# Kernel tuning notes

Measured on AMD Instinct MI355X. Metric: run time of the kernel, lower is better.

## Reference

```python
import jax, jax.numpy as jnp
import numpy as np

N = 50000
E = 800000
F_IN = 128
HID = 64
OUT = 64
H = 4
NEG_SLOPE = 0.2


def setup_inputs() -> dict:
    key = jax.random.key(0)
    ks = jax.random.split(key, 10)
    s = lambda fan_in: 1.0 / np.sqrt(fan_in)
    x = jax.random.normal(ks[0], (N, F_IN), dtype=jnp.float32)
    edge_index = jax.random.randint(ks[1], (2, E), 0, N, dtype=jnp.int64)
    # layer 1: in -> hid, heads H, concat=False
    W1 = jax.random.normal(ks[2], (F_IN, H * HID), dtype=jnp.float32) * s(F_IN)
    a_src1 = jax.random.normal(ks[3], (H, HID), dtype=jnp.float32) * s(HID)
    a_dst1 = jax.random.normal(ks[4], (H, HID), dtype=jnp.float32) * s(HID)
    b1 = jnp.zeros((HID,), dtype=jnp.float32)
    # layer 2: hid -> out
    W2 = jax.random.normal(ks[5], (HID, H * OUT), dtype=jnp.float32) * s(HID)
    a_src2 = jax.random.normal(ks[6], (H, OUT), dtype=jnp.float32) * s(OUT)
    a_dst2 = jax.random.normal(ks[7], (H, OUT), dtype=jnp.float32) * s(OUT)
    b2 = jnp.zeros((OUT,), dtype=jnp.float32)
    return {"x": x, "edge_index": edge_index, "W1": W1, "a_src1": a_src1,
            "a_dst1": a_dst1, "b1": b1, "W2": W2, "a_src2": a_src2,
            "a_dst2": a_dst2, "b2": b2}


def gat_layer(x, src, dst, W, a_s, a_d, b):
    n, h, c = x.shape[0], a_s.shape[0], a_s.shape[1]
    hfeat = (x @ W).reshape(n, h, c)                      # [N,H,C]
    # per-node attention halves, gathered per edge
    alpha_src = jnp.einsum('nhc,hc->nh', hfeat, a_s)       # [N,H]
    alpha_dst = jnp.einsum('nhc,hc->nh', hfeat, a_d)
    e = alpha_src[src] + alpha_dst[dst]                    # [E,H]
    e = jnp.where(e >= 0, e, NEG_SLOPE * e)                # LeakyReLU(0.2)
    # segment softmax over destination node neighborhoods
    m = jax.ops.segment_max(e, dst, num_segments=n)
    e = jnp.exp(e - m[dst])
    denom = jax.ops.segment_sum(e, dst, num_segments=n)
    alpha = e / (denom[dst] + 1e-16)                       # [E,H]
    msg = hfeat[src] * alpha[:, :, None]                   # [E,H,C]
    out = jax.ops.segment_sum(msg, dst, num_segments=n)    # [N,H,C]
    return out.mean(axis=1) + b                            # concat=False -> head mean


def reference(x, edge_index, W1, a_src1, a_dst1, b1, W2, a_src2, a_dst2, b2):
    src, dst = edge_index[0], edge_index[1]
    h = gat_layer(x, src, dst, W1, a_src1, a_dst1, b1)
    h = jax.nn.relu(h)
    h = gat_layer(h, src, dst, W2, a_src2, a_dst2, b2)
    return jax.nn.log_softmax(h, axis=1)
```

## Files before the change

kernel.cpp:

```cpp
#include <hip/hip_runtime.h>
#include <math.h>

constexpr int NNODE = 50000;
constexpr int FIN   = 128;
constexpr int HID   = 64;
constexpr int NH    = 4;
constexpr int NC    = 256;
constexpr float NEG = 0.2f;
constexpr int MPAD  = 50048;
constexpr int SCANB = (NNODE + 255) / 256;

typedef unsigned short u16;
typedef unsigned int   u32;
typedef __fp16 h16x8 __attribute__((ext_vector_type(8)));
typedef __fp16 h2    __attribute__((ext_vector_type(2)));
typedef float  f32x4 __attribute__((ext_vector_type(4)));

__device__ __forceinline__ u16 f2h(float f) {
  union { __fp16 h; u16 u; } c; c.h = (__fp16)f; return c.u;
}
__device__ __forceinline__ h2 u2h2(u32 u) {
  union { u32 u; h2 h; } c; c.u = u; return c.h;
}
__device__ __forceinline__ float readlane_f(float v, int l) {
  return __int_as_float(__builtin_amdgcn_readlane(__float_as_int(v), l));
}
__device__ __forceinline__ u32 h2bf8(u16 hx) {
  return ((u32)hx + 0x7Fu + ((hx >> 8) & 1u)) >> 8;
}

__global__ __launch_bounds__(256) void pack_zero(const float* __restrict__ W1,
                                                 const float* __restrict__ W2,
                                                 u16* __restrict__ Bp1, u16* __restrict__ Bp2,
                                                 int* __restrict__ deg, int packBlocks, int n) {
  int b = blockIdx.x;
  if (b < packBlocks) {
    int i = b * 256 + threadIdx.x;
    const int t1 = FIN * NC;
    const int t2 = HID * NC;
    if (i < t1) {
      int k = i >> 8, c = i & 255;
      Bp1[((size_t)(k >> 3) * 256 + c) * 8 + (k & 7)] = f2h(W1[i]);
    } else if (i < t1 + t2) {
      int j = i - t1;
      int k = j >> 8, c = j & 255;
      Bp2[((size_t)(k >> 3) * 256 + c) * 8 + (k & 7)] = f2h(W2[j]);
    }
  } else {
    int i = (b - packBlocks) * 256 + threadIdx.x;
    if (i < n) deg[i] = 0;
  }
}

__global__ __launch_bounds__(256) void scan_phase1(const int* __restrict__ deg,
                                                   int* __restrict__ blockSums, int n) {
  __shared__ int sm[256];
  int tid = threadIdx.x;
  int i = blockIdx.x * 256 + tid;
  sm[tid] = (i < n) ? deg[i] : 0;
  __syncthreads();
#pragma unroll
  for (int o = 128; o > 0; o >>= 1) {
    if (tid < o) sm[tid] += sm[tid + o];
    __syncthreads();
  }
  if (tid == 0) blockSums[blockIdx.x] = sm[0];
}

__global__ __launch_bounds__(256) void scan_phase23(const int* __restrict__ blockSums,
                                                    const int* __restrict__ deg,
                                                    int* __restrict__ offs, int n) {
  __shared__ int ss[256];
  __shared__ int sm[256];
  int tid = threadIdx.x;
  ss[tid] = (tid < SCANB) ? blockSums[tid] : 0;
  __syncthreads();
#pragma unroll
  for (int o = 1; o < 256; o <<= 1) {
    int t = (tid >= o) ? ss[tid - o] : 0;
    __syncthreads();
    ss[tid] += t;
    __syncthreads();
  }
  int blockOff = (blockIdx.x == 0) ? 0 : ss[blockIdx.x - 1];
  int i = blockIdx.x * 256 + tid;
  int v = (i < n) ? deg[i] : 0;
  sm[tid] = v;
  __syncthreads();
#pragma unroll
  for (int o = 1; o < 256; o <<= 1) {
    int t = (tid >= o) ? sm[tid - o] : 0;
    __syncthreads();
    sm[tid] += t;
    __syncthreads();
  }
  int ex = sm[tid] - v + blockOff;
  if (i < n) offs[i] = ex;
  if (blockIdx.x == SCANB - 1 && tid == 255) offs[n] = ss[SCANB - 1];
}

template <int KS, bool AF32, bool F8>
__device__ __forceinline__ void gemm_body(
    int bx, const void* __restrict__ Aptr, const u16* __restrict__ Bp,
    const float* __restrict__ a_s, const float* __restrict__ a_d,
    void* __restrict__ feat, float* __restrict__ al_s, float* __restrict__ al_d, int M) {
  const int K = 32 * KS;
  int lane = threadIdx.x & 63;
  int wv = threadIdx.x >> 6;
  int q = lane >> 4, r = lane & 15;
  int m0 = bx * 64 + wv * 16;

  h16x8 af[KS];
  if (AF32) {
    int ar = m0 + r; if (ar >= M) ar = M - 1;
    const float* arow = (const float*)Aptr + (size_t)ar * K + q * 8;
#pragma unroll
    for (int ks = 0; ks < KS; ++ks) {
      float4 v0 = *(const float4*)(arow + ks * 32);
      float4 v1 = *(const float4*)(arow + ks * 32 + 4);
      union { h16x8 v; h2 p[4]; } u;
      u.p[0] = __builtin_amdgcn_cvt_pkrtz(v0.x, v0.y);
      u.p[1] = __builtin_amdgcn_cvt_pkrtz(v0.z, v0.w);
      u.p[2] = __builtin_amdgcn_cvt_pkrtz(v1.x, v1.y);
      u.p[3] = __builtin_amdgcn_cvt_pkrtz(v1.z, v1.w);
      af[ks] = u.v;
    }
  } else {
    const u16* arow = (const u16*)Aptr + (size_t)(m0 + r) * K + q * 8;
#pragma unroll
    for (int ks = 0; ks < KS; ++ks) af[ks] = *(const h16x8*)(arow + ks * 32);
  }

  int node_base = m0 + q * 4;
  u32 pk8[4][4];
  if (F8) {
#pragma unroll
    for (int a = 0; a < 4; ++a)
#pragma unroll
      for (int b = 0; b < 4; ++b) pk8[a][b] = 0u;
  }
#pragma unroll
  for (int h = 0; h < NH; ++h) {
    f32x4 acc[4];
#pragma unroll
    for (int c4 = 0; c4 < 4; ++c4) {
      acc[c4] = (f32x4){0.f, 0.f, 0.f, 0.f};
      const u16* bp = Bp + ((size_t)q * 256 + (h * 4 + c4) * 16 + r) * 8;
#pragma unroll
      for (int ks = 0; ks < KS; ++ks) {
        h16x8 bf = *(const h16x8*)(bp + (size_t)ks * 4 * 256 * 8);
        acc[c4] = __builtin_amdgcn_mfma_f32_16x16x32_f16(af[ks], bf, acc[c4], 0, 0, 0);
      }
    }
    float ps[4] = {0.f, 0.f, 0.f, 0.f}, pd[4] = {0.f, 0.f, 0.f, 0.f};
#pragma unroll
    for (int c4 = 0; c4 < 4; ++c4) {
      float sa = a_s[h * HID + c4 * 16 + r];
      float da = a_d[h * HID + c4 * 16 + r];
#pragma unroll
      for (int reg = 0; reg < 4; ++reg) {
        float v = acc[c4][reg];
        ps[reg] += v * sa;
        pd[reg] += v * da;
        if (F8) {
          pk8[c4][reg] |= h2bf8(f2h(v)) << (8 * h);
        } else {
          int node = node_base + reg;
          if (node < M) ((u16*)feat)[(size_t)node * NC + (c4 * 16 + r) * NH + h] = f2h(v);
        }
      }
    }
#pragma unroll
    for (int reg = 0; reg < 4; ++reg) {
#pragma unroll
      for (int o = 1; o < 16; o <<= 1) {
        ps[reg] += __shfl_xor(ps[reg], o);
        pd[reg] += __shfl_xor(pd[reg], o);
      }
      int node = node_base + reg;
      if (r == 0 && node < M) {
        al_s[node * NH + h] = ps[reg];
        al_d[node * NH + h] = pd[reg];
      }
    }
  }
  if (F8) {
#pragma unroll
    for (int c4 = 0; c4 < 4; ++c4)
#pragma unroll
      for (int reg = 0; reg < 4; ++reg) {
        int node = node_base + reg;
        if (node < M)
          *(u32*)((char*)feat + (size_t)node * 256 + (c4 * 16 + r) * 4) = pk8[c4][reg];
      }
  }
}

__global__ __launch_bounds__(256) void count_gemm1(
    const float* __restrict__ x, const u16* __restrict__ Bp1,
    const float* __restrict__ a_s, const float* __restrict__ a_d,
    void* __restrict__ hf8, float* __restrict__ al_s, float* __restrict__ al_d, int M,
    const int* __restrict__ ei, int* __restrict__ deg, int* __restrict__ rank,
    int E, int gemmBlocks) {
  int b = blockIdx.x;
  if (b < gemmBlocks) {
    gemm_body<4, true, true>(b, x, Bp1, a_s, a_d, hf8, al_s, al_d, M);
  } else {
    int i = (b - gemmBlocks) * 256 + threadIdx.x;
    if (i < E) rank[i] = atomicAdd(&deg[ei[E + i]], 1);
  }
}

__global__ __launch_bounds__(256) void scatter_kernel(
    const int* __restrict__ ei, const int* __restrict__ offs,
    const int* __restrict__ rank, int* __restrict__ csr_src, int E) {
  int i = blockIdx.x * 256 + threadIdx.x;
  if (i < E) {
    int dst = ei[E + i];
    csr_src[offs[dst] + rank[i]] = ei[i];
  }
}

__global__ __launch_bounds__(256) void gemm2_kernel(
    const u16* __restrict__ h1bf, const u16* __restrict__ Bp2,
    const float* __restrict__ a_s, const float* __restrict__ a_d,
    void* __restrict__ hf8, float* __restrict__ al_s, float* __restrict__ al_d, int M) {
  gemm_body<2, false, true>(blockIdx.x, h1bf, Bp2, a_s, a_d, hf8, al_s, al_d, M);
}

template <bool FINAL, bool F8>
__global__ __launch_bounds__(256) void agg_kernel(const void* __restrict__ feat,
                                                  const float4* __restrict__ al_s4,
                                                  const float4* __restrict__ al_d4,
                                                  const int* __restrict__ offs,
                                                  const int* __restrict__ csr,
                                                  const float* __restrict__ bias,
                                                  void* __restrict__ out_v, int n) {
  int lane = threadIdx.x & 63;
  int node = blockIdx.x * 4 + (threadIdx.x >> 6);
  if (node >= n) return;
  float4 ad = al_d4[node];
  int lj = lane & 7;
  int hsel = (lane >> 3) & 3;
  float adv = hsel == 0 ? ad.x : (hsel == 1 ? ad.y : (hsel == 2 ? ad.z : ad.w));
  h2 acc01 = {(__fp16)0.f, (__fp16)0.f};
  h2 acc23 = {(__fp16)0.f, (__fp16)0.f};
  float dacc = 0.f;
  int s = offs[node], e = offs[node + 1];
  int nch = (e - s + 7) >> 3;
  int i = s;
  int voff = F8 ? lane * 4 : lane * 8;

  int vidx = 0;
  float4 as = make_float4(0.f, 0.f, 0.f, 0.f);
  uint2 hv[8];
  if (nch > 0) {
    int id0 = i + lj; if (id0 >= e) id0 = e - 1;
    vidx = csr[id0];
    as = al_s4[vidx];
#pragma unroll
    for (int j = 0; j < 8; ++j) {
      int sa = __builtin_amdgcn_readlane(vidx, j);
      if (F8) hv[j].x = *(const u32*)((const char*)feat + (size_t)sa * 256 + voff);
      else    hv[j]   = *(const uint2*)((const char*)feat + (size_t)sa * 512 + voff);
    }
  }

  for (int ch = 0; ch < nch; ++ch) {
    bool last = (ch + 1 == nch);
    float asv = hsel == 0 ? as.x : (hsel == 1 ? as.y : (hsel == 2 ? as.z : as.w));
    float ev = asv + adv;
    ev = ev >= 0.f ? ev : NEG * ev;
    float wv = __expf(ev - 1.3862944f);
    if (i + lj >= e) wv = 0.f;
    float t = wv;
    t += __shfl_xor(t, 1); t += __shfl_xor(t, 2); t += __shfl_xor(t, 4);
    dacc += t;
    float w8 = __shfl_xor(wv, 8);
    union { h2 h; u32 u; } pc;
    pc.h = __builtin_amdgcn_cvt_pkrtz(wv, w8);
    int vidx_n = 0;
    float4 as_n = make_float4(0.f, 0.f, 0.f, 0.f);
    uint2 hn[8];
    if (!last) {
      int id1 = i + 8 + lj; if (id1 >= e) id1 = e - 1;
      vidx_n = csr[id1];
      as_n = al_s4[vidx_n];
#pragma unroll
      for (int j = 0; j < 8; ++j) {
        int sa = __builtin_amdgcn_readlane(vidx_n, j);
        if (F8) hn[j].x = *(const u32*)((const char*)feat + (size_t)sa * 256 + voff);
        else    hn[j]   = *(const uint2*)((const char*)feat + (size_t)sa * 512 + voff);
      }
    }
#pragma unroll
    for (int j = 0; j < 8; ++j) {
      u32 w01 = (u32)__builtin_amdgcn_readlane((int)pc.u, j);
      u32 w23 = (u32)__builtin_amdgcn_readlane((int)pc.u, 16 + j);
      u32 f01, f23;
      if (F8) {
        f01 = __builtin_amdgcn_perm(0u, hv[j].x, 0x01080008u);
        f23 = __builtin_amdgcn_perm(0u, hv[j].x, 0x03080208u);
      } else {
        f01 = hv[j].x; f23 = hv[j].y;
      }
      acc01 += u2h2(w01) * u2h2(f01);
      acc23 += u2h2(w23) * u2h2(f23);
    }
    if (!last) {
      vidx = vidx_n; as = as_n;
#pragma unroll
      for (int j = 0; j < 8; ++j) hv[j] = hn[j];
    }
    i += 8;
  }
  float d0 = readlane_f(dacc, 0), d1 = readlane_f(dacc, 8);
  float d2 = readlane_f(dacc, 16), d3 = readlane_f(dacc, 24);
  float val = 0.25f * ((float)acc01.x / (d0 + 1e-16f) + (float)acc01.y / (d1 + 1e-16f) +
                       (float)acc23.x / (d2 + 1e-16f) + (float)acc23.y / (d3 + 1e-16f)) +
              bias[lane];
  if (!FINAL) {
    ((u16*)out_v)[(size_t)node * HID + lane] = f2h(fmaxf(val, 0.f));
  } else {
    float mx = val;
#pragma unroll
    for (int o = 32; o >= 1; o >>= 1) mx = fmaxf(mx, __shfl_xor(mx, o));
    float ex = __expf(val - mx);
    float sm = ex;
#pragma unroll
    for (int o = 32; o >= 1; o >>= 1) sm += __shfl_xor(sm, o);
    ((float*)out_v)[(size_t)node * HID + lane] = (val - mx) - logf(sm);
  }
}

extern "C" void kernel_launch(void* const* d_in, const int* in_sizes, int n_in,
                              void* d_out, int out_size, void* d_ws, size_t ws_size,
                              hipStream_t stream) {
  const float* x   = (const float*)d_in[0];
  const int*   ei  = (const int*)d_in[1];
  const float* W1  = (const float*)d_in[2];
  const float* as1 = (const float*)d_in[3];
  const float* ad1 = (const float*)d_in[4];
  const float* b1  = (const float*)d_in[5];
  const float* W2  = (const float*)d_in[6];
  const float* as2 = (const float*)d_in[7];
  const float* ad2 = (const float*)d_in[8];
  const float* b2  = (const float*)d_in[9];
  float* out = (float*)d_out;

  const int N = NNODE;
  const int E = in_sizes[1] / 2;

  char* base = (char*)d_ws;
  size_t off = 0;
  auto alloc = [&](size_t bytes) -> void* {
    void* p = base + off;
    off += (bytes + 255) & ~(size_t)255;
    return p;
  };
  u32*    hf8    = (u32*)alloc((size_t)N * 256);
  u16*    h1bf   = (u16*)alloc((size_t)MPAD * HID * 2);
  u16*    Bp1    = (u16*)alloc((size_t)FIN * NC * 2);
  u16*    Bp2    = (u16*)alloc((size_t)HID * NC * 2);
  float*  al_s   = (float*)alloc((size_t)N * NH * 4);
  float*  al_d   = (float*)alloc((size_t)N * NH * 4);
  int*    deg    = (int*)alloc((size_t)N * 4);
  int*    offs   = (int*)alloc((size_t)(N + 1) * 4);
  int*    rank   = (int*)alloc((size_t)E * 4);
  int*    csr    = (int*)alloc((size_t)(E + 16) * 4);
  int*    bsums  = (int*)alloc(256 * 4);

  const int edgeBlocks = (E + 255) / 256;
  const int gemmBlocks = MPAD / 64;
  const int nodeBlocks = (N + 3) / 4;
  const int packBlocks = (FIN * NC + HID * NC + 255) / 256;

  pack_zero<<<packBlocks + SCANB, 256, 0, stream>>>(W1, W2, Bp1, Bp2, deg, packBlocks, N);

  count_gemm1<<<gemmBlocks + edgeBlocks, 256, 0, stream>>>(
      x, Bp1, as1, ad1, hf8, al_s, al_d, N,
      ei, deg, rank, E, gemmBlocks);

  scan_phase1<<<SCANB, 256, 0, stream>>>(deg, bsums, N);
  scan_phase23<<<SCANB, 256, 0, stream>>>(bsums, deg, offs, N);
  scatter_kernel<<<edgeBlocks, 256, 0, stream>>>(ei, offs, rank, csr, E);

  agg_kernel<false, true><<<nodeBlocks, 256, 0, stream>>>(hf8, (const float4*)al_s, (const float4*)al_d,
                                                          offs, csr, b1, h1bf, N);

  gemm2_kernel<<<gemmBlocks, 256, 0, stream>>>(h1bf, Bp2, as2, ad2, hf8, al_s, al_d, N);
  agg_kernel<true, true><<<nodeBlocks, 256, 0, stream>>>(hf8, (const float4*)al_s, (const float4*)al_d,
                                                         offs, csr, b2, out, N);
}
```

Baseline: 248.1 us.

## Replicate degree counters to spread atomics and merge scan into one kernel

Degree counting now spreads its atomics over four replicated counter arrays, picked by edge block index, to reduce contention on hot destination nodes. A single scan kernel replaces the two-phase scan: each block recomputes all block sums redundantly and also writes per-copy offsets that the scatter uses for CSR positions. This removes one launch and lowers atomic contention, in exchange for a larger zeroing pass, extra offset storage, and redundant whole-array reads in every scan block.

```diff
diff --git a/kernel.cpp b/kernel.cpp
--- a/kernel.cpp
+++ b/kernel.cpp
@@ -9,6 +9,7 @@
 constexpr float NEG = 0.2f;
 constexpr int MPAD  = 50048;
 constexpr int SCANB = (NNODE + 255) / 256;
+constexpr int NCPY  = 4;
 
 typedef unsigned short u16;
 typedef unsigned int   u32;
@@ -32,7 +33,7 @@
 __global__ __launch_bounds__(256) void pack_zero(const float* __restrict__ W1,
                                                  const float* __restrict__ W2,
                                                  u16* __restrict__ Bp1, u16* __restrict__ Bp2,
-                                                 int* __restrict__ deg, int packBlocks, int n) {
+                                                 int* __restrict__ deg4, int packBlocks, int n) {
   int b = blockIdx.x;
   if (b < packBlocks) {
     int i = b * 256 + threadIdx.x;
@@ -48,55 +49,8 @@
     }
   } else {
     int i = (b - packBlocks) * 256 + threadIdx.x;
-    if (i < n) deg[i] = 0;
-  }
-}
-
-__global__ __launch_bounds__(256) void scan_phase1(const int* __restrict__ deg,
-                                                   int* __restrict__ blockSums, int n) {
-  __shared__ int sm[256];
-  int tid = threadIdx.x;
-  int i = blockIdx.x * 256 + tid;
-  sm[tid] = (i < n) ? deg[i] : 0;
-  __syncthreads();
-#pragma unroll
-  for (int o = 128; o > 0; o >>= 1) {
-    if (tid < o) sm[tid] += sm[tid + o];
-    __syncthreads();
-  }
-  if (tid == 0) blockSums[blockIdx.x] = sm[0];
-}
-
-__global__ __launch_bounds__(256) void scan_phase23(const int* __restrict__ blockSums,
-                                                    const int* __restrict__ deg,
-                                                    int* __restrict__ offs, int n) {
-  __shared__ int ss[256];
-  __shared__ int sm[256];
-  int tid = threadIdx.x;
-  ss[tid] = (tid < SCANB) ? blockSums[tid] : 0;
-  __syncthreads();
-#pragma unroll
-  for (int o = 1; o < 256; o <<= 1) {
-    int t = (tid >= o) ? ss[tid - o] : 0;
-    __syncthreads();
-    ss[tid] += t;
-    __syncthreads();
-  }
-  int blockOff = (blockIdx.x == 0) ? 0 : ss[blockIdx.x - 1];
-  int i = blockIdx.x * 256 + tid;
-  int v = (i < n) ? deg[i] : 0;
-  sm[tid] = v;
-  __syncthreads();
-#pragma unroll
-  for (int o = 1; o < 256; o <<= 1) {
-    int t = (tid >= o) ? sm[tid - o] : 0;
-    __syncthreads();
-    sm[tid] += t;
-    __syncthreads();
-  }
-  int ex = sm[tid] - v + blockOff;
-  if (i < n) offs[i] = ex;
-  if (blockIdx.x == SCANB - 1 && tid == 255) offs[n] = ss[SCANB - 1];
+    if (i < NCPY * n) deg4[i] = 0;
+  }
 }
 
 template <int KS, bool AF32, bool F8>
@@ -200,24 +154,83 @@
     const float* __restrict__ x, const u16* __restrict__ Bp1,
     const float* __restrict__ a_s, const float* __restrict__ a_d,
     void* __restrict__ hf8, float* __restrict__ al_s, float* __restrict__ al_d, int M,
-    const int* __restrict__ ei, int* __restrict__ deg, int* __restrict__ rank,
+    const int* __restrict__ ei, int* __restrict__ deg4, int* __restrict__ rank,
     int E, int gemmBlocks) {
   int b = blockIdx.x;
   if (b < gemmBlocks) {
     gemm_body<4, true, true>(b, x, Bp1, a_s, a_d, hf8, al_s, al_d, M);
   } else {
-    int i = (b - gemmBlocks) * 256 + threadIdx.x;
-    if (i < E) rank[i] = atomicAdd(&deg[ei[E + i]], 1);
+    int b2 = b - gemmBlocks;
+    int i = b2 * 256 + threadIdx.x;
+    int c = b2 & (NCPY - 1);
+    if (i < E) rank[i] = atomicAdd(&deg4[(size_t)c * NNODE + ei[E + i]], 1);
+  }
+}
+
+__global__ __launch_bounds__(256) void scan_all(const int* __restrict__ deg4,
+                                                int* __restrict__ offs,
+                                                int* __restrict__ coff, int n) {
+  __shared__ int ss[256];
+  __shared__ int wsum[SCANB * 4];
+  int tid = threadIdx.x;
+  int wv = tid >> 6, ln = tid & 63;
+  for (int k = 0; k < SCANB; ++k) {
+    int idx = k * 256 + tid;
+    int v = 0;
+    if (idx < n)
+      v = deg4[idx] + deg4[n + idx] + deg4[2 * n + idx] + deg4[3 * n + idx];
+#pragma unroll
+    for (int o = 1; o < 64; o <<= 1) v += __shfl_xor(v, o);
+    if (ln == 0) wsum[k * 4 + wv] = v;
+  }
+  __syncthreads();
+  ss[tid] = 0;
+  if (tid < SCANB)
+    ss[tid] = wsum[tid * 4] + wsum[tid * 4 + 1] + wsum[tid * 4 + 2] + wsum[tid * 4 + 3];
+  __syncthreads();
+#pragma unroll
+  for (int o = 1; o < 256; o <<= 1) {
+    int t = (tid >= o) ? ss[tid - o] : 0;
+    __syncthreads();
+    ss[tid] += t;
+    __syncthreads();
+  }
+  int blockOff = (blockIdx.x == 0) ? 0 : ss[blockIdx.x - 1];
+  int i = blockIdx.x * 256 + tid;
+  int d0 = 0, d1 = 0, d2 = 0, d3 = 0;
+  if (i < n) {
+    d0 = deg4[i]; d1 = deg4[n + i]; d2 = deg4[2 * n + i]; d3 = deg4[3 * n + i];
+  }
+  int tot = d0 + d1 + d2 + d3;
+  __syncthreads();
+  ss[tid] = tot;
+  __syncthreads();
+#pragma unroll
+  for (int o = 1; o < 256; o <<= 1) {
+    int t = (tid >= o) ? ss[tid - o] : 0;
+    __syncthreads();
+    ss[tid] += t;
+    __syncthreads();
+  }
+  int ex = ss[tid] - tot + blockOff;
+  if (i < n) {
+    offs[i] = ex;
+    coff[i] = ex;
+    coff[n + i] = ex + d0;
+    coff[2 * n + i] = ex + d0 + d1;
+    coff[3 * n + i] = ex + d0 + d1 + d2;
+    if (i == n - 1) offs[n] = ex + tot;
   }
 }
 
 __global__ __launch_bounds__(256) void scatter_kernel(
-    const int* __restrict__ ei, const int* __restrict__ offs,
+    const int* __restrict__ ei, const int* __restrict__ coff,
     const int* __restrict__ rank, int* __restrict__ csr_src, int E) {
   int i = blockIdx.x * 256 + threadIdx.x;
   if (i < E) {
+    int c = (i >> 8) & (NCPY - 1);
     int dst = ei[E + i];
-    csr_src[offs[dst] + rank[i]] = ei[i];
+    csr_src[coff[(size_t)c * NNODE + dst] + rank[i]] = ei[i];
   }
 }
 
@@ -364,26 +377,27 @@
   u16*    Bp2    = (u16*)alloc((size_t)HID * NC * 2);
   float*  al_s   = (float*)alloc((size_t)N * NH * 4);
   float*  al_d   = (float*)alloc((size_t)N * NH * 4);
-  int*    deg    = (int*)alloc((size_t)N * 4);
+  int*    deg4   = (int*)alloc((size_t)NCPY * N * 4);
+  int*    coff   = (int*)alloc((size_t)NCPY * N * 4);
   int*    offs   = (int*)alloc((size_t)(N + 1) * 4);
   int*    rank   = (int*)alloc((size_t)E * 4);
   int*    csr    = (int*)alloc((size_t)(E + 16) * 4);
-  int*    bsums  = (int*)alloc(256 * 4);
 
   const int edgeBlocks = (E + 255) / 256;
   const int gemmBlocks = MPAD / 64;
   const int nodeBlocks = (N + 3) / 4;
   const int packBlocks = (FIN * NC + HID * NC + 255) / 256;
-
-  pack_zero<<<packBlocks + SCANB, 256, 0, stream>>>(W1, W2, Bp1, Bp2, deg, packBlocks, N);
+  const int zeroBlocks = (NCPY * N + 255) / 256;
+
+  pack_zero<<<packBlocks + zeroBlocks, 256, 0, stream>>>(W1, W2, Bp1, Bp2, deg4, packBlocks, N);
 
   count_gemm1<<<gemmBlocks + edgeBlocks, 256, 0, stream>>>(
       x, Bp1, as1, ad1, hf8, al_s, al_d, N,
-      ei, deg, rank, E, gemmBlocks);
-
-  scan_phase1<<<SCANB, 256, 0, stream>>>(deg, bsums, N);
-  scan_phase23<<<SCANB, 256, 0, stream>>>(bsums, deg, offs, N);
-  scatter_kernel<<<edgeBlocks, 256, 0, stream>>>(ei, offs, rank, csr, E);
+      ei, deg4, rank, E, gemmBlocks);
+
+  scan_all<<<SCANB, 256, 0, stream>>>(deg4, offs, coff, N);
+
+  scatter_kernel<<<edgeBlocks, 256, 0, stream>>>(ei, coff, rank, csr, E);
 
   agg_kernel<false, true><<<nodeBlocks, 256, 0, stream>>>(hf8, (const float4*)al_s, (const float4*)al_d,
                                                           offs, csr, b1, h1bf, N);
```

Measured after the change: 328.0 us. 32.2% more time.
